# Optimization experiments

Hardware: AMD Instinct MI355X
Metric: run time of the kernel (lower is better)

## Reference

```python
import jax, jax.numpy as jnp
import numpy as np

B, S, D = 2, 2048, 1024
H, HKV = 16, 4
HD = D // H          # 64
NREP = H // HKV      # 4
EPS = 1e-6
ROPE_BASE = 10000.0


def setup_inputs() -> dict:
    key = jax.random.key(0)
    ks = jax.random.split(key, 6)
    std = 0.02
    return {
        "x": jax.random.normal(ks[0], (B, S, D), dtype=jnp.float32),
        "Wq": jax.random.normal(ks[1], (D, H * HD), dtype=jnp.float32) * std,
        "Wk": jax.random.normal(ks[2], (D, HKV * HD), dtype=jnp.float32) * std,
        "Wv": jax.random.normal(ks[3], (D, HKV * HD), dtype=jnp.float32) * std,
        "Wo": jax.random.normal(ks[4], (D, D), dtype=jnp.float32) * std,
        "norm_w": jnp.ones((D,), dtype=jnp.float32),
    }


def _rope_cos_sin(seq_len, head_dim, dtype):
    inv_freq = 1.0 / (ROPE_BASE ** (jnp.arange(0, head_dim, 2, dtype=jnp.float32) / head_dim))
    t = jnp.arange(seq_len, dtype=jnp.float32)
    freqs = jnp.outer(t, inv_freq)                 # [S, HD/2]
    emb = jnp.concatenate([freqs, freqs], axis=-1)  # [S, HD]
    return jnp.cos(emb).astype(dtype), jnp.sin(emb).astype(dtype)


def _rotate_half(x):
    x1, x2 = jnp.split(x, 2, axis=-1)
    return jnp.concatenate([-x2, x1], axis=-1)


def _apply_rope(x, cos, sin):
    # x: [B, nh, S, HD]; cos/sin: [S, HD]
    return x * cos[None, None] + _rotate_half(x) * sin[None, None]


def reference(x, Wq, Wk, Wv, Wo, norm_w):
    b, s, _ = x.shape
    q = (x @ Wq).reshape(b, s, H, HD).transpose(0, 2, 1, 3)      # [B,H,S,HD]
    k = (x @ Wk).reshape(b, s, HKV, HD).transpose(0, 2, 1, 3)    # [B,HKV,S,HD]
    v = (x @ Wv).reshape(b, s, HKV, HD).transpose(0, 2, 1, 3)

    cos, sin = _rope_cos_sin(s, HD, x.dtype)
    q = _apply_rope(q, cos, sin)
    k = _apply_rope(k, cos, sin)

    # repeat kv heads to match q heads
    k = jnp.repeat(k, NREP, axis=1)   # [B,H,S,HD]
    v = jnp.repeat(v, NREP, axis=1)

    scale = HD ** -0.5
    scores = jnp.einsum('bhqd,bhkd->bhqk', q, k) * scale   # [B,H,S,S]
    attn = jax.nn.softmax(scores, axis=-1)
    out = jnp.einsum('bhqk,bhkd->bhqd', attn, v)            # [B,H,S,HD]
    out = out.transpose(0, 2, 1, 3).reshape(b, s, D)
    out = out @ Wo

    # RMSNorm
    rms = jnp.sqrt(jnp.mean(out * out, axis=-1, keepdims=True) + EPS)
    out = out / rms * norm_w
    return out
```

## Files before the change

### kernel.cpp

```cpp
#include <hip/hip_runtime.h>
#include <hip/hip_bf16.h>
#include <stdint.h>
#include <math.h>

typedef __bf16 bf16x8 __attribute__((ext_vector_type(8)));
typedef float f32x4 __attribute__((ext_vector_type(4)));
typedef float f32x16 __attribute__((ext_vector_type(16)));

#define B_    2
#define S_    2048
#define D_    1024
#define H_    16
#define HKV_  4
#define HD_   64
#define MTOT  4096
#define NQKV  1536
#define BHS   65536

#define ZERO16 {0.f,0.f,0.f,0.f,0.f,0.f,0.f,0.f,0.f,0.f,0.f,0.f,0.f,0.f,0.f,0.f}

__device__ __forceinline__ unsigned short f2bf(float f) {
  union { float f; unsigned u; } v; v.f = f;
  unsigned r = (v.u + 0x7FFFu + ((v.u >> 16) & 1u)) >> 16;
  return (unsigned short)r;
}

__device__ __forceinline__ float bf2f(unsigned short u) {
  union { unsigned u; float f; } v; v.u = (unsigned)u << 16; return v.f;
}

__device__ __forceinline__ float fast_exp2(float x) {
  return __builtin_amdgcn_exp2f(x);
}

__device__ __forceinline__ unsigned cvt_pk_bf16(float lo, float hi) {
  unsigned r;
  asm("v_cvt_pk_bf16_f32 %0, %1, %2" : "=v"(r) : "v"(lo), "v"(hi));
  return r;
}

__device__ __forceinline__ void gl_lds16(const void* g, void* l) {
  __builtin_amdgcn_global_load_lds((const __attribute__((address_space(1))) void*)g,
                                   (__attribute__((address_space(3))) void*)l, 16, 0, 0);
}

__global__ __launch_bounds__(256) void k_pre(const float* __restrict__ Wq, const float* __restrict__ Wk,
                                             const float* __restrict__ Wv, const float* __restrict__ Wo,
                                             const float* __restrict__ x,
                                             unsigned short* __restrict__ wqkvt,
                                             unsigned short* __restrict__ wot,
                                             unsigned short* __restrict__ xb,
                                             float* __restrict__ cost, float* __restrict__ sint) {
  int bid = blockIdx.x, tid = threadIdx.x;
  if (bid < 640) {
    const float* src; unsigned short* dst; int ldsrc, cb, rb;
    if (bid < 256)      { src = Wq; dst = wqkvt;                          ldsrc = 1024; cb = (bid & 15) * 64; rb = (bid >> 4) * 64; }
    else if (bid < 320) { int i = bid - 256; src = Wk; dst = wqkvt + (size_t)1024 * 1024; ldsrc = 256; cb = (i & 3) * 64; rb = (i >> 2) * 64; }
    else if (bid < 384) { int i = bid - 320; src = Wv; dst = wqkvt + (size_t)1280 * 1024; ldsrc = 256; cb = (i & 3) * 64; rb = (i >> 2) * 64; }
    else                { int i = bid - 384; src = Wo; dst = wot;         ldsrc = 1024; cb = (i & 15) * 64; rb = (i >> 4) * 64; }
    __shared__ unsigned short T[64][72];
    for (int rep = 0; rep < 4; ++rep) {
      int idx = rep * 256 + tid;
      int r = idx >> 4, seg = idx & 15;
      float4 v = *(const float4*)&src[(size_t)(rb + r) * ldsrc + cb + seg * 4];
      T[seg*4+0][r] = f2bf(v.x);
      T[seg*4+1][r] = f2bf(v.y);
      T[seg*4+2][r] = f2bf(v.z);
      T[seg*4+3][r] = f2bf(v.w);
    }
    __syncthreads();
    for (int rep = 0; rep < 2; ++rep) {
      int idx = rep * 256 + tid;
      int c = idx >> 3, seg = idx & 7;
      *(uint4*)&dst[(size_t)(cb + c) * 1024 + rb + seg * 8] = *(const uint4*)&T[c][seg * 8];
    }
  } else if (bid < 896) {
    int idx = (bid - 640) * 256 + tid;
    int s = idx >> 5, i = idx & 31;
    double inv = exp(-(double)i / 32.0 * log(10000.0));
    double ang = (double)s * inv;
    cost[idx] = (float)cos(ang);
    sint[idx] = (float)sin(ang);
  } else {
    int i = (bid - 896) * 256 + tid;
    const int n4 = MTOT * D_ / 4;
    for (; i < n4; i += 1024 * 256) {
      float4 v = ((const float4*)x)[i];
      ushort4 o;
      o.x = f2bf(v.x); o.y = f2bf(v.y); o.z = f2bf(v.z); o.w = f2bf(v.w);
      ((ushort4*)xb)[i] = o;
    }
  }
}

__global__ __launch_bounds__(256) void k_gemm_bt(const unsigned short* __restrict__ A,
                                                 const unsigned short* __restrict__ Bt,
                                                 unsigned short* __restrict__ C0,
                                                 unsigned short* __restrict__ C1,
                                                 int M, int N, int Kfull) {
  int nb = blockIdx.x, mb = blockIdx.y, z = blockIdx.z;
  int kbase = z * (Kfull >> 1);
  int Klen = Kfull >> 1;
  unsigned short* C = z ? C1 : C0;
  __shared__ unsigned short As[2][128 * 32];
  __shared__ unsigned short Bs[2][128 * 32];
  int tid = threadIdx.x, lane = tid & 63, w = tid >> 6;
  int wr = w >> 1, wc = w & 1;
  f32x4 acc[4][4];
  for (int m = 0; m < 4; ++m) for (int n = 0; n < 4; ++n) acc[m][n] = (f32x4){0.f, 0.f, 0.f, 0.f};

  const int r16 = lane >> 2;
  const int c8  = (lane & 3) * 8;

  auto stage = [&](int buf, int kt) {
    for (int j = 0; j < 2; ++j) {
      int rbase = (w * 2 + j) * 16;
      gl_lds16(&A [(size_t)(mb * 128 + rbase + r16) * Kfull + kbase + kt * 32 + c8], &As[buf][rbase * 32]);
      gl_lds16(&Bt[(size_t)(nb * 128 + rbase + r16) * Kfull + kbase + kt * 32 + c8], &Bs[buf][rbase * 32]);
    }
  };
  stage(0, 0);
  int NT = Klen / 32;
  int cur = 0;
  const int lr = lane & 15, lg8 = (lane >> 4) * 8;
  for (int kt = 0; kt < NT; ++kt) {
    __syncthreads();
    if (kt + 1 < NT) stage(cur ^ 1, kt + 1);
    bf16x8 af[4], bfr[4];
    for (int m = 0; m < 4; ++m) af[m]  = *(const bf16x8*)&As[cur][(wr * 64 + m * 16 + lr) * 32 + lg8];
    for (int n = 0; n < 4; ++n) bfr[n] = *(const bf16x8*)&Bs[cur][(wc * 64 + n * 16 + lr) * 32 + lg8];
    for (int m = 0; m < 4; ++m)
      for (int n = 0; n < 4; ++n)
        acc[m][n] = __builtin_amdgcn_mfma_f32_16x16x32_bf16(af[m], bfr[n], acc[m][n], 0, 0, 0);
    cur ^= 1;
  }
  int lq = (lane >> 4) * 4;
  for (int m = 0; m < 4; ++m)
    for (int n = 0; n < 4; ++n)
      for (int r = 0; r < 4; ++r)
        C[(size_t)(mb * 128 + wr * 64 + m * 16 + lq + r) * N + nb * 128 + wc * 64 + n * 16 + lr] =
            f2bf(acc[m][n][r]);
}

__global__ __launch_bounds__(256) void k_rope_v(const unsigned short* __restrict__ qp0,
                                                const unsigned short* __restrict__ qp1,
                                                const float* __restrict__ cost,
                                                const float* __restrict__ sint,
                                                unsigned short* __restrict__ Qb,
                                                unsigned short* __restrict__ Kb,
                                                unsigned short* __restrict__ Vt) {
  int bid = blockIdx.x, tid = threadIdx.x;
  if (bid < MTOT) {
    int blk = bid;
    int b = blk >> 11, s = blk & 2047;
    const unsigned short* r0 = qp0 + (size_t)blk * NQKV;
    const unsigned short* r1 = qp1 + (size_t)blk * NQKV;
    const float QSCALE = 0.18033688011112042f;
    {
      int e = tid * 4;
      int h = e >> 6, d = e & 63, d2 = d & 31;
      float4 cs = *(const float4*)&cost[s * 32 + d2];
      float4 sn = *(const float4*)&sint[s * 32 + d2];
      ushort4 a0 = *(const ushort4*)&r0[e],      a1 = *(const ushort4*)&r1[e];
      ushort4 b0 = *(const ushort4*)&r0[e ^ 32], b1 = *(const ushort4*)&r1[e ^ 32];
      float ax = bf2f(a0.x) + bf2f(a1.x), ay = bf2f(a0.y) + bf2f(a1.y);
      float az = bf2f(a0.z) + bf2f(a1.z), aw = bf2f(a0.w) + bf2f(a1.w);
      float bx = bf2f(b0.x) + bf2f(b1.x), by = bf2f(b0.y) + bf2f(b1.y);
      float bz = bf2f(b0.z) + bf2f(b1.z), bw = bf2f(b0.w) + bf2f(b1.w);
      float sgn = (d < 32) ? -1.f : 1.f;
      ushort4 o;
      o.x = f2bf((ax * cs.x + sgn * bx * sn.x) * QSCALE);
      o.y = f2bf((ay * cs.y + sgn * by * sn.y) * QSCALE);
      o.z = f2bf((az * cs.z + sgn * bz * sn.z) * QSCALE);
      o.w = f2bf((aw * cs.w + sgn * bw * sn.w) * QSCALE);
      *(ushort4*)&Qb[(((size_t)(b * H_ + h)) * S_ + s) * HD_ + d] = o;
    }
    if (tid < 64) {
      int e = tid * 4;
      int hk = e >> 6, d = e & 63, d2 = d & 31;
      float4 cs = *(const float4*)&cost[s * 32 + d2];
      float4 sn = *(const float4*)&sint[s * 32 + d2];
      ushort4 a0 = *(const ushort4*)&r0[1024 + e],        a1 = *(const ushort4*)&r1[1024 + e];
      ushort4 b0 = *(const ushort4*)&r0[1024 + (e ^ 32)], b1 = *(const ushort4*)&r1[1024 + (e ^ 32)];
      float ax = bf2f(a0.x) + bf2f(a1.x), ay = bf2f(a0.y) + bf2f(a1.y);
      float az = bf2f(a0.z) + bf2f(a1.z), aw = bf2f(a0.w) + bf2f(a1.w);
      float bx = bf2f(b0.x) + bf2f(b1.x), by = bf2f(b0.y) + bf2f(b1.y);
      float bz = bf2f(b0.z) + bf2f(b1.z), bw = bf2f(b0.w) + bf2f(b1.w);
      float sgn = (d < 32) ? -1.f : 1.f;
      ushort4 o;
      o.x = f2bf(ax * cs.x + sgn * bx * sn.x);
      o.y = f2bf(ay * cs.y + sgn * by * sn.y);
      o.z = f2bf(az * cs.z + sgn * bz * sn.z);
      o.w = f2bf(aw * cs.w + sgn * bw * sn.w);
      *(ushort4*)&Kb[(((size_t)(b * HKV_ + hk)) * S_ + s) * HD_ + d] = o;
    }
  } else {
    int i = bid - MTOT;
    int sb = (i & 31) * 64;
    int yy = i >> 5;
    int b = yy >> 2, hk = yy & 3;
    __shared__ unsigned short T[64][72];
    for (int rep = 0; rep < 4; ++rep) {
      int idx = rep * 256 + tid;
      int r = idx >> 4, seg = idx & 15;
      size_t off = ((size_t)(b * S_ + sb + r)) * NQKV + 1280 + hk * 64 + seg * 4;
      ushort4 a0 = *(const ushort4*)&qp0[off];
      ushort4 a1 = *(const ushort4*)&qp1[off];
      T[seg*4+0][r] = f2bf(bf2f(a0.x) + bf2f(a1.x));
      T[seg*4+1][r] = f2bf(bf2f(a0.y) + bf2f(a1.y));
      T[seg*4+2][r] = f2bf(bf2f(a0.z) + bf2f(a1.z));
      T[seg*4+3][r] = f2bf(bf2f(a0.w) + bf2f(a1.w));
    }
    __syncthreads();
    for (int rep = 0; rep < 2; ++rep) {
      int idx = rep * 256 + tid;
      int d = idx >> 3, seg = idx & 7;
      *(uint4*)&Vt[(((size_t)(b * HKV_ + hk)) * HD_ + d) * S_ + sb + seg * 8] = *(const uint4*)&T[d][seg * 8];
    }
  }
}

__global__ __launch_bounds__(512, 2) void k_attn(const unsigned short* __restrict__ Q,
                                                 const unsigned short* __restrict__ K,
                                                 const unsigned short* __restrict__ Vt,
                                                 unsigned short* __restrict__ Ob) {
  int qt = blockIdx.x;
  int bh = blockIdx.y;
  int b = bh >> 4, h = bh & 15, hk = h >> 2;
  const unsigned short* Qp = Q + (((size_t)(b * H_ + h)) * S_ + qt * 128) * HD_;
  const unsigned short* Kp = K + ((size_t)(b * HKV_ + hk)) * S_ * HD_;
  const unsigned short* Vp = Vt + ((size_t)(b * HKV_ + hk)) * HD_ * S_;

  __shared__ unsigned short Lds[2 * 16384];

  const int tid = threadIdx.x, lane = tid & 63, w = tid >> 6;
  const int g  = w >> 2;
  const int wl = w & 3;
  const int col = lane & 31;
  const int hi  = lane >> 5;
  const int sw  = lane & 7;
  const int kv0 = g * (S_ / 2);
  const int gbase = g * 16384;

  const unsigned short* pka[4];
  #pragma unroll
  for (int kc = 0; kc < 4; ++kc)
    pka[kc] = &Lds[gbase + col * 64 + ((kc * 2 + hi) ^ sw) * 8];

  bf16x8 qf[4];
  {
    const unsigned short* qrow = Qp + (size_t)(wl * 32 + col) * HD_;
    #pragma unroll
    for (int dc = 0; dc < 4; ++dc)
      qf[dc] = *(const bf16x8*)&qrow[dc * 16 + hi * 8];
  }

  union { unsigned short s[8]; bf16x8 v; } onesu;
  #pragma unroll
  for (int i = 0; i < 8; ++i) onesu.s[i] = 0x3F80;
  const bf16x8 ones = onesu.v;

  f32x16 oacc0 = ZERO16, oacc1 = ZERO16, lacc = ZERO16;

  const int rl = lane >> 3, cs = lane & 7;
  const int row0 = wl * 16 + rl;
  const int csrc = (cs ^ (row0 & 7)) * 8;
  const unsigned short* srcK = &Kp[(size_t)(kv0 + row0) * HD_ + csrc];
  const unsigned short* srcV = &Vp[(size_t)row0 * S_ + kv0 + csrc];

  auto stage = [&](int be) {
    gl_lds16(srcK,           &Lds[gbase + be + (wl * 16) * 64]);
    gl_lds16(srcK + 8 * HD_, &Lds[gbase + be + (wl * 16 + 8) * 64]);
    gl_lds16(srcV,           &Lds[gbase + be + 8192 + (wl * 16) * 64]);
    gl_lds16(srcV + 8 * S_,  &Lds[gbase + be + 8192 + (wl * 16 + 8) * 64]);
    srcK += 64 * HD_;
    srcV += 64;
  };

  auto compute = [&](int be) {
    bf16x8 pf[4];
    #pragma unroll
    for (int blk2 = 0; blk2 < 2; ++blk2) {
      f32x16 st = ZERO16;
      __builtin_amdgcn_s_setprio(1);
      #pragma unroll
      for (int kc = 0; kc < 4; ++kc) {
        bf16x8 kf = *(const bf16x8*)(pka[kc] + be + blk2 * 2048);
        st = __builtin_amdgcn_mfma_f32_32x32x16_bf16(kf, qf[kc], st, 0, 0, 0);
      }
      __builtin_amdgcn_s_setprio(0);
      #pragma unroll
      for (int i = 0; i < 16; ++i)
        st[i] = fast_exp2(st[i]);
      #pragma unroll
      for (int kcl = 0; kcl < 2; ++kcl) {
        int base = kcl * 8;
        unsigned u0 = cvt_pk_bf16(st[base + 0], st[base + 1]);
        unsigned u1 = cvt_pk_bf16(st[base + 2], st[base + 3]);
        unsigned u2 = cvt_pk_bf16(st[base + 4], st[base + 5]);
        unsigned u3 = cvt_pk_bf16(st[base + 6], st[base + 7]);
        asm("v_permlane32_swap_b32 %0, %1" : "+v"(u0), "+v"(u2));
        asm("v_permlane32_swap_b32 %0, %1" : "+v"(u1), "+v"(u3));
        union { unsigned u[4]; bf16x8 v; } pk;
        pk.u[0] = u0; pk.u[1] = u1; pk.u[2] = u2; pk.u[3] = u3;
        pf[blk2 * 2 + kcl] = pk.v;
      }
    }
    __builtin_amdgcn_s_setprio(1);
    #pragma unroll
    for (int kc = 0; kc < 4; ++kc)
      lacc = __builtin_amdgcn_mfma_f32_32x32x16_bf16(ones, pf[kc], lacc, 0, 0, 0);
    #pragma unroll
    for (int kc = 0; kc < 4; ++kc) {
      bf16x8 v0 = *(const bf16x8*)(pka[kc] + be + 8192);
      bf16x8 v1 = *(const bf16x8*)(pka[kc] + be + 8192 + 2048);
      oacc0 = __builtin_amdgcn_mfma_f32_32x32x16_bf16(v0, pf[kc], oacc0, 0, 0, 0);
      oacc1 = __builtin_amdgcn_mfma_f32_32x32x16_bf16(v1, pf[kc], oacc1, 0, 0, 0);
    }
    __builtin_amdgcn_s_setprio(0);
  };

  stage(0);
  for (int it = 0; it < 8; ++it) {
    __syncthreads();
    stage(4096);
    compute(0);
    __syncthreads();
    if (it < 7) stage(0);
    compute(4096);
  }

  __syncthreads();
  float* xch = (float*)Lds;
  if (g == 0) {
    float* slot = xch + ((size_t)wl * 64 + lane) * 33;
    #pragma unroll
    for (int i = 0; i < 16; ++i) { slot[i] = oacc0[i]; slot[16 + i] = oacc1[i]; }
    slot[32] = lacc[0];
  }
  __syncthreads();
  if (g == 1) {
    const float* slot = xch + ((size_t)wl * 64 + lane) * 33;
    float rinv = 1.f / (lacc[0] + slot[32]);
    int qrow = qt * 128 + wl * 32 + col;
    unsigned short* ob = Ob + ((size_t)(b * S_ + qrow)) * D_ + h * 64;
    #pragma unroll
    for (int rr = 0; rr < 4; ++rr) {
      ushort4 o0, o1;
      o0.x = f2bf((oacc0[rr*4+0] + slot[rr*4+0]) * rinv);
      o0.y = f2bf((oacc0[rr*4+1] + slot[rr*4+1]) * rinv);
      o0.z = f2bf((oacc0[rr*4+2] + slot[rr*4+2]) * rinv);
      o0.w = f2bf((oacc0[rr*4+3] + slot[rr*4+3]) * rinv);
      o1.x = f2bf((oacc1[rr*4+0] + slot[16+rr*4+0]) * rinv);
      o1.y = f2bf((oacc1[rr*4+1] + slot[16+rr*4+1]) * rinv);
      o1.z = f2bf((oacc1[rr*4+2] + slot[16+rr*4+2]) * rinv);
      o1.w = f2bf((oacc1[rr*4+3] + slot[16+rr*4+3]) * rinv);
      *(ushort4*)&ob[8 * rr + 4 * hi]      = o0;
      *(ushort4*)&ob[32 + 8 * rr + 4 * hi] = o1;
    }
  }
}

__global__ __launch_bounds__(256) void k_rmsnorm(const unsigned short* __restrict__ in0,
                                                 const unsigned short* __restrict__ in1,
                                                 const float* __restrict__ wt,
                                                 float* __restrict__ out) {
  int row = blockIdx.x, tid = threadIdx.x;
  ushort4 u0 = *(const ushort4*)&in0[(size_t)row * D_ + tid * 4];
  ushort4 u1 = *(const ushort4*)&in1[(size_t)row * D_ + tid * 4];
  float x0 = bf2f(u0.x) + bf2f(u1.x);
  float x1 = bf2f(u0.y) + bf2f(u1.y);
  float x2 = bf2f(u0.z) + bf2f(u1.z);
  float x3 = bf2f(u0.w) + bf2f(u1.w);
  float ss = x0 * x0 + x1 * x1 + x2 * x2 + x3 * x3;
  for (int o = 32; o >= 1; o >>= 1) ss += __shfl_xor(ss, o);
  __shared__ float red[4];
  if ((tid & 63) == 0) red[tid >> 6] = ss;
  __syncthreads();
  float tot = red[0] + red[1] + red[2] + red[3];
  float rinv = 1.f / sqrtf(tot * (1.f / 1024.f) + 1e-6f);
  float4 wv = ((const float4*)wt)[tid];
  float4 o;
  o.x = x0 * rinv * wv.x;
  o.y = x1 * rinv * wv.y;
  o.z = x2 * rinv * wv.z;
  o.w = x3 * rinv * wv.w;
  ((float4*)(out + (size_t)row * D_))[tid] = o;
}

extern "C" void kernel_launch(void* const* d_in, const int* in_sizes, int n_in,
                              void* d_out, int out_size, void* d_ws, size_t ws_size,
                              hipStream_t stream) {
  const float* x  = (const float*)d_in[0];
  const float* Wq = (const float*)d_in[1];
  const float* Wk = (const float*)d_in[2];
  const float* Wv = (const float*)d_in[3];
  const float* Wo = (const float*)d_in[4];
  const float* nw = (const float*)d_in[5];
  float* out = (float*)d_out;

  char* p = (char*)d_ws;
  unsigned short* xb    = (unsigned short*)p; p += (size_t)MTOT * D_ * 2;
  char*           slot  = p;                  p += (size_t)18 * 1024 * 1024;
  unsigned short* wqkvt = (unsigned short*)p; p += (size_t)NQKV * D_ * 2;
  unsigned short* wot   = (unsigned short*)p; p += (size_t)D_ * D_ * 2;
  unsigned short* qb    = (unsigned short*)p; p += (size_t)B_ * H_ * S_ * HD_ * 2;
  unsigned short* kb    = (unsigned short*)p; p += (size_t)B_ * HKV_ * S_ * HD_ * 2;
  unsigned short* vtb   = (unsigned short*)p; p += (size_t)B_ * HKV_ * HD_ * S_ * 2;
  char*           big2  = p;                  p += (size_t)MTOT * D_ * 2 * 2;
  float*          mlold = (float*)p;          p += (size_t)2 * BHS * 4;
  float*          cost  = (float*)p;          p += (size_t)S_ * 32 * 4;
  float*          sint  = (float*)p;          p += (size_t)S_ * 32 * 4;
  (void)mlold;

  unsigned short* qkv_p0  = (unsigned short*)slot;
  unsigned short* qkv_p1  = (unsigned short*)big2;
  unsigned short* attnb   = (unsigned short*)big2;
  unsigned short* proj_p0 = (unsigned short*)slot;
  unsigned short* proj_p1 = (unsigned short*)(slot + (size_t)MTOT * D_ * 2);

  k_pre<<<1920, 256, 0, stream>>>(Wq, Wk, Wv, Wo, x, wqkvt, wot, xb, cost, sint);

  k_gemm_bt<<<dim3(NQKV / 128, MTOT / 128, 2), 256, 0, stream>>>(xb, wqkvt, qkv_p0, qkv_p1, MTOT, NQKV, D_);
  k_rope_v<<<MTOT + 256, 256, 0, stream>>>(qkv_p0, qkv_p1, cost, sint, qb, kb, vtb);
  k_attn<<<dim3(S_ / 128, B_ * H_), 512, 0, stream>>>(qb, kb, vtb, attnb);
  k_gemm_bt<<<dim3(D_ / 128, MTOT / 128, 2), 256, 0, stream>>>(attnb, wot, proj_p0, proj_p1, MTOT, D_, D_);
  k_rmsnorm<<<MTOT, 256, 0, stream>>>(proj_p0, proj_p1, nw, out);
}
```

Before: 105.8 us.

## Fuse RoPE, Q scaling and V transpose into QKV GEMM epilogue; remap attention grid

Replaces the split-K QKV GEMM and the separate RoPE/V-transpose kernel with one full-K GEMM. Its epilogue applies RoPE to Q and K in registers, using the partner half from acc[n^2], and transposes V through shared memory before writing Vt. This removes the two bf16 partial-sum round trips through global memory and one kernel launch. The attention launch becomes a 1D grid with a swizzled block index, so that blocks sharing KV heads are scheduled closer together. The trade-off is fewer GEMM blocks (no K split) and strided scalar stores for the Q and K outputs.

```diff
diff --git a/kernel.cpp b/kernel.cpp
--- a/kernel.cpp
+++ b/kernel.cpp
@@ -93,6 +93,109 @@
   }
 }
 
+__global__ __launch_bounds__(256) void k_gemm_qkv(const unsigned short* __restrict__ A,
+                                                  const unsigned short* __restrict__ Bt,
+                                                  const float* __restrict__ cost,
+                                                  const float* __restrict__ sint,
+                                                  unsigned short* __restrict__ Qb,
+                                                  unsigned short* __restrict__ Kb,
+                                                  unsigned short* __restrict__ Vt) {
+  int nb = blockIdx.x, mb = blockIdx.y;
+  __shared__ unsigned short Arena[128 * 136];
+  unsigned short* As = Arena;
+  unsigned short* Bs = Arena + 2 * 4096;
+  int tid = threadIdx.x, lane = tid & 63, w = tid >> 6;
+  int wr = w >> 1, wc = w & 1;
+  f32x4 acc[4][4];
+  for (int m = 0; m < 4; ++m) for (int n = 0; n < 4; ++n) acc[m][n] = (f32x4){0.f, 0.f, 0.f, 0.f};
+
+  const int r16 = lane >> 2;
+  const int c8  = (lane & 3) * 8;
+
+  auto stage = [&](int buf, int kt) {
+    for (int j = 0; j < 2; ++j) {
+      int rbase = (w * 2 + j) * 16;
+      gl_lds16(&A [(size_t)(mb * 128 + rbase + r16) * D_ + kt * 32 + c8], &As[buf * 4096 + rbase * 32]);
+      gl_lds16(&Bt[(size_t)(nb * 128 + rbase + r16) * D_ + kt * 32 + c8], &Bs[buf * 4096 + rbase * 32]);
+    }
+  };
+  stage(0, 0);
+  const int NT = D_ / 32;
+  int cur = 0;
+  const int lr = lane & 15, lg8 = (lane >> 4) * 8;
+  for (int kt = 0; kt < NT; ++kt) {
+    __syncthreads();
+    if (kt + 1 < NT) stage(cur ^ 1, kt + 1);
+    bf16x8 af[4], bfr[4];
+    for (int m = 0; m < 4; ++m) af[m]  = *(const bf16x8*)&As[cur * 4096 + (wr * 64 + m * 16 + lr) * 32 + lg8];
+    for (int n = 0; n < 4; ++n) bfr[n] = *(const bf16x8*)&Bs[cur * 4096 + (wc * 64 + n * 16 + lr) * 32 + lg8];
+    for (int m = 0; m < 4; ++m)
+      for (int n = 0; n < 4; ++n)
+        acc[m][n] = __builtin_amdgcn_mfma_f32_16x16x32_bf16(af[m], bfr[n], acc[m][n], 0, 0, 0);
+    cur ^= 1;
+  }
+
+  const int lq = (lane >> 4) * 4;
+  const int b = mb >> 4;
+  const int s0 = (mb & 15) * 128;
+
+  if (nb < 10) {
+    const float QSCALE = 0.18033688011112042f;
+    float scl = (nb < 8) ? QSCALE : 1.f;
+    #pragma unroll
+    for (int m = 0; m < 4; ++m) {
+      #pragma unroll
+      for (int n = 0; n < 4; ++n) {
+        int gc = nb * 128 + wc * 64 + n * 16 + lr;
+        int d  = gc & 63, d2 = d & 31;
+        float sgn = (d < 32) ? -1.f : 1.f;
+        unsigned short* dst;
+        if (nb < 8) {
+          int h = gc >> 6;
+          dst = Qb + (((size_t)(b * H_ + h)) * S_) * HD_ + d;
+        } else {
+          int hk = (gc - 1024) >> 6;
+          dst = Kb + (((size_t)(b * HKV_ + hk)) * S_) * HD_ + d;
+        }
+        #pragma unroll
+        for (int r = 0; r < 4; ++r) {
+          int s = s0 + wr * 64 + m * 16 + lq + r;
+          float c  = cost[s * 32 + d2];
+          float sn = sint[s * 32 + d2];
+          float xv = acc[m][n][r];
+          float xp = acc[m][n ^ 2][r];
+          float o = (xv * c + sgn * xp * sn) * scl;
+          dst[(size_t)s * HD_] = f2bf(o);
+        }
+      }
+    }
+  } else {
+    __syncthreads();
+    #pragma unroll
+    for (int m = 0; m < 4; ++m)
+      #pragma unroll
+      for (int n = 0; n < 4; ++n)
+        #pragma unroll
+        for (int r = 0; r < 4; ++r) {
+          int c = wc * 64 + n * 16 + lr;
+          int rw = wr * 64 + m * 16 + lq + r;
+          Arena[c * 136 + rw] = f2bf(acc[m][n][r]);
+        }
+    __syncthreads();
+    for (int rep = 0; rep < 2; ++rep) {
+      int idx = rep * 256 + tid;
+      int j = idx >> 2, q = idx & 3;
+      int v_off = (nb - 10) * 128 + j;
+      int hk = v_off >> 6, dl = v_off & 63;
+      unsigned short* dst = Vt + (((size_t)(b * HKV_ + hk)) * HD_ + dl) * S_ + s0 + q * 32;
+      const unsigned short* srcp = &Arena[j * 136 + q * 32];
+      #pragma unroll
+      for (int k2 = 0; k2 < 4; ++k2)
+        *(uint4*)&dst[k2 * 8] = *(const uint4*)&srcp[k2 * 8];
+    }
+  }
+}
+
 __global__ __launch_bounds__(256) void k_gemm_bt(const unsigned short* __restrict__ A,
                                                  const unsigned short* __restrict__ Bt,
                                                  unsigned short* __restrict__ C0,
@@ -142,90 +245,13 @@
             f2bf(acc[m][n][r]);
 }
 
-__global__ __launch_bounds__(256) void k_rope_v(const unsigned short* __restrict__ qp0,
-                                                const unsigned short* __restrict__ qp1,
-                                                const float* __restrict__ cost,
-                                                const float* __restrict__ sint,
-                                                unsigned short* __restrict__ Qb,
-                                                unsigned short* __restrict__ Kb,
-                                                unsigned short* __restrict__ Vt) {
-  int bid = blockIdx.x, tid = threadIdx.x;
-  if (bid < MTOT) {
-    int blk = bid;
-    int b = blk >> 11, s = blk & 2047;
-    const unsigned short* r0 = qp0 + (size_t)blk * NQKV;
-    const unsigned short* r1 = qp1 + (size_t)blk * NQKV;
-    const float QSCALE = 0.18033688011112042f;
-    {
-      int e = tid * 4;
-      int h = e >> 6, d = e & 63, d2 = d & 31;
-      float4 cs = *(const float4*)&cost[s * 32 + d2];
-      float4 sn = *(const float4*)&sint[s * 32 + d2];
-      ushort4 a0 = *(const ushort4*)&r0[e],      a1 = *(const ushort4*)&r1[e];
-      ushort4 b0 = *(const ushort4*)&r0[e ^ 32], b1 = *(const ushort4*)&r1[e ^ 32];
-      float ax = bf2f(a0.x) + bf2f(a1.x), ay = bf2f(a0.y) + bf2f(a1.y);
-      float az = bf2f(a0.z) + bf2f(a1.z), aw = bf2f(a0.w) + bf2f(a1.w);
-      float bx = bf2f(b0.x) + bf2f(b1.x), by = bf2f(b0.y) + bf2f(b1.y);
-      float bz = bf2f(b0.z) + bf2f(b1.z), bw = bf2f(b0.w) + bf2f(b1.w);
-      float sgn = (d < 32) ? -1.f : 1.f;
-      ushort4 o;
-      o.x = f2bf((ax * cs.x + sgn * bx * sn.x) * QSCALE);
-      o.y = f2bf((ay * cs.y + sgn * by * sn.y) * QSCALE);
-      o.z = f2bf((az * cs.z + sgn * bz * sn.z) * QSCALE);
-      o.w = f2bf((aw * cs.w + sgn * bw * sn.w) * QSCALE);
-      *(ushort4*)&Qb[(((size_t)(b * H_ + h)) * S_ + s) * HD_ + d] = o;
-    }
-    if (tid < 64) {
-      int e = tid * 4;
-      int hk = e >> 6, d = e & 63, d2 = d & 31;
-      float4 cs = *(const float4*)&cost[s * 32 + d2];
-      float4 sn = *(const float4*)&sint[s * 32 + d2];
-      ushort4 a0 = *(const ushort4*)&r0[1024 + e],        a1 = *(const ushort4*)&r1[1024 + e];
-      ushort4 b0 = *(const ushort4*)&r0[1024 + (e ^ 32)], b1 = *(const ushort4*)&r1[1024 + (e ^ 32)];
-      float ax = bf2f(a0.x) + bf2f(a1.x), ay = bf2f(a0.y) + bf2f(a1.y);
-      float az = bf2f(a0.z) + bf2f(a1.z), aw = bf2f(a0.w) + bf2f(a1.w);
-      float bx = bf2f(b0.x) + bf2f(b1.x), by = bf2f(b0.y) + bf2f(b1.y);
-      float bz = bf2f(b0.z) + bf2f(b1.z), bw = bf2f(b0.w) + bf2f(b1.w);
-      float sgn = (d < 32) ? -1.f : 1.f;
-      ushort4 o;
-      o.x = f2bf(ax * cs.x + sgn * bx * sn.x);
-      o.y = f2bf(ay * cs.y + sgn * by * sn.y);
-      o.z = f2bf(az * cs.z + sgn * bz * sn.z);
-      o.w = f2bf(aw * cs.w + sgn * bw * sn.w);
-      *(ushort4*)&Kb[(((size_t)(b * HKV_ + hk)) * S_ + s) * HD_ + d] = o;
-    }
-  } else {
-    int i = bid - MTOT;
-    int sb = (i & 31) * 64;
-    int yy = i >> 5;
-    int b = yy >> 2, hk = yy & 3;
-    __shared__ unsigned short T[64][72];
-    for (int rep = 0; rep < 4; ++rep) {
-      int idx = rep * 256 + tid;
-      int r = idx >> 4, seg = idx & 15;
-      size_t off = ((size_t)(b * S_ + sb + r)) * NQKV + 1280 + hk * 64 + seg * 4;
-      ushort4 a0 = *(const ushort4*)&qp0[off];
-      ushort4 a1 = *(const ushort4*)&qp1[off];
-      T[seg*4+0][r] = f2bf(bf2f(a0.x) + bf2f(a1.x));
-      T[seg*4+1][r] = f2bf(bf2f(a0.y) + bf2f(a1.y));
-      T[seg*4+2][r] = f2bf(bf2f(a0.z) + bf2f(a1.z));
-      T[seg*4+3][r] = f2bf(bf2f(a0.w) + bf2f(a1.w));
-    }
-    __syncthreads();
-    for (int rep = 0; rep < 2; ++rep) {
-      int idx = rep * 256 + tid;
-      int d = idx >> 3, seg = idx & 7;
-      *(uint4*)&Vt[(((size_t)(b * HKV_ + hk)) * HD_ + d) * S_ + sb + seg * 8] = *(const uint4*)&T[d][seg * 8];
-    }
-  }
-}
-
 __global__ __launch_bounds__(512, 2) void k_attn(const unsigned short* __restrict__ Q,
                                                  const unsigned short* __restrict__ K,
                                                  const unsigned short* __restrict__ Vt,
                                                  unsigned short* __restrict__ Ob) {
-  int qt = blockIdx.x;
-  int bh = blockIdx.y;
+  int wg = ((blockIdx.x & 7) << 6) | (blockIdx.x >> 3);
+  int qt = wg & 15;
+  int bh = wg >> 4;
   int b = bh >> 4, h = bh & 15, hk = h >> 2;
   const unsigned short* Qp = Q + (((size_t)(b * H_ + h)) * S_ + qt * 128) * HD_;
   const unsigned short* Kp = K + ((size_t)(b * HKV_ + hk)) * S_ * HD_;
@@ -413,17 +439,14 @@
   float*          sint  = (float*)p;          p += (size_t)S_ * 32 * 4;
   (void)mlold;
 
-  unsigned short* qkv_p0  = (unsigned short*)slot;
-  unsigned short* qkv_p1  = (unsigned short*)big2;
   unsigned short* attnb   = (unsigned short*)big2;
   unsigned short* proj_p0 = (unsigned short*)slot;
   unsigned short* proj_p1 = (unsigned short*)(slot + (size_t)MTOT * D_ * 2);
 
   k_pre<<<1920, 256, 0, stream>>>(Wq, Wk, Wv, Wo, x, wqkvt, wot, xb, cost, sint);
 
-  k_gemm_bt<<<dim3(NQKV / 128, MTOT / 128, 2), 256, 0, stream>>>(xb, wqkvt, qkv_p0, qkv_p1, MTOT, NQKV, D_);
-  k_rope_v<<<MTOT + 256, 256, 0, stream>>>(qkv_p0, qkv_p1, cost, sint, qb, kb, vtb);
-  k_attn<<<dim3(S_ / 128, B_ * H_), 512, 0, stream>>>(qb, kb, vtb, attnb);
+  k_gemm_qkv<<<dim3(NQKV / 128, MTOT / 128), 256, 0, stream>>>(xb, wqkvt, cost, sint, qb, kb, vtb);
+  k_attn<<<512, 512, 0, stream>>>(qb, kb, vtb, attnb);
   k_gemm_bt<<<dim3(D_ / 128, MTOT / 128, 2), 256, 0, stream>>>(attnb, wot, proj_p0, proj_p1, MTOT, D_, D_);
   k_rmsnorm<<<MTOT, 256, 0, stream>>>(proj_p0, proj_p1, nw, out);
 }
```

New measurement: 103.1 us. -2.6%, faster.
